# Kernel optimization log

Measured on AMD Instinct MI355X. Metric: run time of the kernel, lower is better.

## Reference

```python
import jax, jax.numpy as jnp
import numpy as np

# physics constants of the two-reaction model
K1 = 1.0
BETA = 16.0
F = 0.1
VR = 1.0
DELTA = 0.01  # sample_time
NG = 3

B, T = 4096, 256
NU, NYS, NUS = 1, 9, 3  # u dim, yseq dim (=(Np-1)*Ng), useq dim (=(Np-1)*Nu)
H = 64
FIN = NG + NYS + NUS  # 15


def setup_inputs() -> dict:
    key = jax.random.key(0)
    ks = jax.random.split(key, 8)
    return {
        "u": jax.random.uniform(ks[0], (B, T, NU), dtype=jnp.float32),
        "yseq": jax.random.uniform(ks[1], (B, T, NYS), dtype=jnp.float32),
        "useq": jax.random.uniform(ks[2], (B, T, NUS), dtype=jnp.float32),
        "W1": 0.1 * jax.random.normal(ks[3], (FIN, H), dtype=jnp.float32),
        "b1": jnp.zeros((H,), jnp.float32),
        "W2": 0.1 * jax.random.normal(ks[4], (H, H), dtype=jnp.float32),
        "b2": jnp.zeros((H,), jnp.float32),
        "W3": 0.1 * jax.random.normal(ks[5], (H, NG), dtype=jnp.float32),
        "b3": jnp.zeros((NG,), jnp.float32),
    }


def _fg(x, u):
    # RHS of the two-reaction ODE; x: (B, 3), u: (B, 1)
    Ca, Cd, Cc = x[..., 0:1], x[..., 1:2], x[..., 2:3]
    Ca0 = u[..., 0:1]
    s = jnp.sqrt(1.0 + BETA * Ca)
    dCa = F * (Ca0 - Ca) / VR - K1 * Ca
    dCd = 0.5 * K1 * Ca * (s - 1.0) / (s + 1.0) - F * Cd / VR
    dCc = 2.0 * K1 * Ca / (1.0 + s) - F * Cc / VR
    return jnp.concatenate([dCa, dCd, dCc], axis=-1)


def reference(u, yseq, useq, W1, b1, W2, b2, W3, b3):
    def fnn(x, ys, us):
        h = jnp.concatenate([x, ys, us], axis=-1)
        h = jax.nn.relu(h @ W1 + b1)
        h = jax.nn.relu(h @ W2 + b2)
        return h @ W3 + b3

    def step(xG, inp):
        u_t, ys_t, us_t = inp
        rhs = lambda x: _fg(x, u_t) + fnn(x, ys_t, us_t)
        k1 = rhs(xG)
        k2 = rhs(xG + 0.5 * DELTA * k1)
        k3 = rhs(xG + 0.5 * DELTA * k2)
        k4 = rhs(xG + DELTA * k3)
        xnext = xG + (DELTA / 6.0) * (k1 + 2.0 * k2 + 2.0 * k3 + k4)
        return xnext, xG  # output y = current state

    x0 = jnp.zeros((u.shape[0], NG), u.dtype)
    xs = (jnp.moveaxis(u, 1, 0), jnp.moveaxis(yseq, 1, 0), jnp.moveaxis(useq, 1, 0))
    _, ys_out = jax.lax.scan(step, x0, xs)
    return jnp.moveaxis(ys_out, 0, 1)  # (B, T, Ng)
```

## Files before the change

kernel.cpp:

```cpp
#include <hip/hip_runtime.h>

#define NB 4096
#define NT 256
#define NH 64


template <int ctrl, int rm, int bm>
__device__ __forceinline__ float dpp_add(float v) {
    int m = __builtin_amdgcn_update_dpp(0, __builtin_bit_cast(int, v),
                                        ctrl, rm, bm, true);
    return v + __builtin_bit_cast(float, m);
}

__device__ __forceinline__ float wave_sum(float v) {
    v = dpp_add<0x111, 0xf, 0xf>(v);
    v = dpp_add<0x112, 0xf, 0xf>(v);
    v = dpp_add<0x114, 0xf, 0xe>(v);
    v = dpp_add<0x118, 0xf, 0xc>(v);
    v = dpp_add<0x142, 0xa, 0xf>(v);
    v = dpp_add<0x143, 0xc, 0xf>(v);
    return __builtin_bit_cast(float,
        __builtin_amdgcn_readlane(__builtin_bit_cast(int, v), 63));
}

__global__ __attribute__((amdgpu_flat_work_group_size(256, 256),
                          amdgpu_waves_per_eu(4, 4)))
void tworeac_kernel(
    const float* __restrict__ u, const float* __restrict__ yseq,
    const float* __restrict__ useq, const float* __restrict__ W1,
    const float* __restrict__ b1, const float* __restrict__ W2,
    const float* __restrict__ b2, const float* __restrict__ W3,
    const float* __restrict__ b3, float* __restrict__ out)
{
    const int lane = threadIdx.x & 63;
    const int wave = threadIdx.x >> 6;
    const int b = blockIdx.x * 4 + wave;

    __shared__ float h1s[4][NH];

    float w1x[3], w1y[9], w1u[3], w2r[NH], w3r[3];
    #pragma unroll
    for (int i = 0; i < 3; ++i) w1x[i] = W1[i * NH + lane];
    #pragma unroll
    for (int i = 0; i < 9; ++i) w1y[i] = W1[(3 + i) * NH + lane];
    #pragma unroll
    for (int i = 0; i < 3; ++i) w1u[i] = W1[(12 + i) * NH + lane];
    #pragma unroll
    for (int j = 0; j < NH; ++j) w2r[j] = W2[j * NH + lane];
    #pragma unroll
    for (int k = 0; k < 3; ++k) w3r[k] = W3[lane * 3 + k];
    #pragma unroll
    for (int j = 0; j < NH; ++j) asm volatile("" : "+v"(w2r[j]));

    const float b1h = b1[lane];
    const float b2h = b2[lane];
    const float b30 = b3[0], b31 = b3[1], b32 = b3[2];

    const float* ub  = u    + (size_t)b * NT;
    const float* ysb = yseq + (size_t)b * NT * 9;
    const float* usb = useq + (size_t)b * NT * 3;
    float*       ob  = out  + (size_t)b * NT * 3;

    float x0 = 0.f, x1 = 0.f, x2 = 0.f;

    float base1 = 0.f, ut = 0.f;
    auto rhs = [&](float xa, float xd, float xc,
                   float& d0, float& d1, float& d2) {
        float h1 = fmaf(xa, w1x[0], fmaf(xd, w1x[1], fmaf(xc, w1x[2], base1)));
        h1 = fmaxf(h1, 0.f);
        h1s[wave][lane] = h1;
        __builtin_amdgcn_wave_barrier();
        float a0 = 0.f, a1 = 0.f, a2 = 0.f, a3 = 0.f;
        #pragma unroll
        for (int j = 0; j < NH / 4; ++j) {
            float4 hv = *reinterpret_cast<const float4*>(&h1s[wave][4 * j]);
            a0 = fmaf(hv.x, w2r[4 * j + 0], a0);
            a1 = fmaf(hv.y, w2r[4 * j + 1], a1);
            a2 = fmaf(hv.z, w2r[4 * j + 2], a2);
            a3 = fmaf(hv.w, w2r[4 * j + 3], a3);
        }
        __builtin_amdgcn_wave_barrier();
        float h2 = fmaxf(b2h + ((a0 + a1) + (a2 + a3)), 0.f);
        float s0 = wave_sum(h2 * w3r[0]);
        float s1 = wave_sum(h2 * w3r[1]);
        float s2 = wave_sum(h2 * w3r[2]);
        float s = sqrtf(fmaf(16.f, xa, 1.f));
        float r = 1.f / (1.f + s);
        d0 = (fmaf(0.1f, ut - xa, -xa)) + s0 + b30;
        d1 = fmaf(0.5f * xa * (s - 1.f), r, -0.1f * xd) + s1 + b31;
        d2 = (2.f * xa * r - 0.1f * xc) + s2 + b32;
    };

    for (int t = 0; t < NT; ++t) {
        if (lane < 3) ob[t * 3 + lane] = (lane == 0) ? x0 : (lane == 1 ? x1 : x2);

        ut = ub[t];
        base1 = b1h;
        #pragma unroll
        for (int i = 0; i < 9; ++i) base1 = fmaf(ysb[t * 9 + i], w1y[i], base1);
        #pragma unroll
        for (int i = 0; i < 3; ++i) base1 = fmaf(usb[t * 3 + i], w1u[i], base1);

        float k0, k1v, k2v, a0, a1, a2;
        rhs(x0, x1, x2, k0, k1v, k2v);
        a0 = k0; a1 = k1v; a2 = k2v;
        rhs(fmaf(0.005f, k0, x0), fmaf(0.005f, k1v, x1),
            fmaf(0.005f, k2v, x2), k0, k1v, k2v);
        a0 = fmaf(2.f, k0, a0); a1 = fmaf(2.f, k1v, a1); a2 = fmaf(2.f, k2v, a2);
        rhs(fmaf(0.005f, k0, x0), fmaf(0.005f, k1v, x1),
            fmaf(0.005f, k2v, x2), k0, k1v, k2v);
        a0 = fmaf(2.f, k0, a0); a1 = fmaf(2.f, k1v, a1); a2 = fmaf(2.f, k2v, a2);
        rhs(fmaf(0.01f, k0, x0), fmaf(0.01f, k1v, x1),
            fmaf(0.01f, k2v, x2), k0, k1v, k2v);
        a0 += k0; a1 += k1v; a2 += k2v;

        const float c = 0.01f / 6.f;
        x0 = fmaf(c, a0, x0);
        x1 = fmaf(c, a1, x1);
        x2 = fmaf(c, a2, x2);
    }
}

extern "C" void kernel_launch(void* const* d_in, const int* in_sizes, int n_in,
                              void* d_out, int out_size, void* d_ws, size_t ws_size,
                              hipStream_t stream) {
    const float* u    = (const float*)d_in[0];
    const float* yseq = (const float*)d_in[1];
    const float* useq = (const float*)d_in[2];
    const float* W1   = (const float*)d_in[3];
    const float* b1   = (const float*)d_in[4];
    const float* W2   = (const float*)d_in[5];
    const float* b2   = (const float*)d_in[6];
    const float* W3   = (const float*)d_in[7];
    const float* b3   = (const float*)d_in[8];
    float* out = (float*)d_out;

    tworeac_kernel<<<NB / 4, 256, 0, stream>>>(u, yseq, useq, W1, b1, W2, b2,
                                               W3, b3, out);
}
```

Measured before the change: 1.187 ms.

## Process two batch chains per wave with packed FP32 math and interleaved reductions

Each wave now integrates two independent batch rows at once, halving the grid. The layer-2 matvec uses packed two-wide float math against the shared W2 registers, and the six wave reductions are interleaved to hide DPP latency. The sqrt and reciprocal calls become the fast hardware intrinsics. The aim is more instruction-level parallelism in the latency-bound serial RK4 chain, at the cost of fewer waves and more registers, with the occupancy hint relaxed to allow that.

```diff
diff --git a/kernel.cpp b/kernel.cpp
--- a/kernel.cpp
+++ b/kernel.cpp
@@ -2,7 +2,8 @@
 
 #define NB 4096
 #define NT 256
-#define NH 64
+
+typedef float f32x2 __attribute__((ext_vector_type(2)));
 
 
 template <int ctrl, int rm, int bm>
@@ -12,19 +13,13 @@
     return v + __builtin_bit_cast(float, m);
 }
 
-__device__ __forceinline__ float wave_sum(float v) {
-    v = dpp_add<0x111, 0xf, 0xf>(v);
-    v = dpp_add<0x112, 0xf, 0xf>(v);
-    v = dpp_add<0x114, 0xf, 0xe>(v);
-    v = dpp_add<0x118, 0xf, 0xc>(v);
-    v = dpp_add<0x142, 0xa, 0xf>(v);
-    v = dpp_add<0x143, 0xc, 0xf>(v);
+__device__ __forceinline__ float rl63(float v) {
     return __builtin_bit_cast(float,
         __builtin_amdgcn_readlane(__builtin_bit_cast(int, v), 63));
 }
 
 __global__ __attribute__((amdgpu_flat_work_group_size(256, 256),
-                          amdgpu_waves_per_eu(4, 4)))
+                          amdgpu_waves_per_eu(2, 4)))
 void tworeac_kernel(
     const float* __restrict__ u, const float* __restrict__ yseq,
     const float* __restrict__ useq, const float* __restrict__ W1,
@@ -34,90 +29,143 @@
 {
     const int lane = threadIdx.x & 63;
     const int wave = threadIdx.x >> 6;
-    const int b = blockIdx.x * 4 + wave;
+    const int cA = (blockIdx.x * 4 + wave) * 2;
+    const int cB = cA + 1;
 
-    __shared__ float h1s[4][NH];
+    __shared__ float h1A[4][64];
+    __shared__ float h1B[4][64];
 
-    float w1x[3], w1y[9], w1u[3], w2r[NH], w3r[3];
+    f32x2 w2p[32];
     #pragma unroll
-    for (int i = 0; i < 3; ++i) w1x[i] = W1[i * NH + lane];
+    for (int m = 0; m < 32; ++m)
+        w2p[m] = (f32x2){W2[(2 * m) * 64 + lane], W2[(2 * m + 1) * 64 + lane]};
+    float w1x[3], w1y[9], w1u[3], w3r[3];
     #pragma unroll
-    for (int i = 0; i < 9; ++i) w1y[i] = W1[(3 + i) * NH + lane];
+    for (int i = 0; i < 3; ++i) w1x[i] = W1[i * 64 + lane];
     #pragma unroll
-    for (int i = 0; i < 3; ++i) w1u[i] = W1[(12 + i) * NH + lane];
+    for (int i = 0; i < 9; ++i) w1y[i] = W1[(3 + i) * 64 + lane];
     #pragma unroll
-    for (int j = 0; j < NH; ++j) w2r[j] = W2[j * NH + lane];
+    for (int i = 0; i < 3; ++i) w1u[i] = W1[(12 + i) * 64 + lane];
     #pragma unroll
     for (int k = 0; k < 3; ++k) w3r[k] = W3[lane * 3 + k];
-    #pragma unroll
-    for (int j = 0; j < NH; ++j) asm volatile("" : "+v"(w2r[j]));
-
     const float b1h = b1[lane];
     const float b2h = b2[lane];
     const float b30 = b3[0], b31 = b3[1], b32 = b3[2];
 
-    const float* ub  = u    + (size_t)b * NT;
-    const float* ysb = yseq + (size_t)b * NT * 9;
-    const float* usb = useq + (size_t)b * NT * 3;
-    float*       ob  = out  + (size_t)b * NT * 3;
+    const float* uA  = u    + (size_t)cA * NT;
+    const float* uB  = u    + (size_t)cB * NT;
+    const float* ysA = yseq + (size_t)cA * NT * 9;
+    const float* ysB = yseq + (size_t)cB * NT * 9;
+    const float* usA = useq + (size_t)cA * NT * 3;
+    const float* usB = useq + (size_t)cB * NT * 3;
+    float*       oA  = out  + (size_t)cA * NT * 3;
+    float*       oB  = out  + (size_t)cB * NT * 3;
 
-    float x0 = 0.f, x1 = 0.f, x2 = 0.f;
+    f32x2 x0p = (f32x2)0.f, x1p = (f32x2)0.f, x2p = (f32x2)0.f;
 
-    float base1 = 0.f, ut = 0.f;
-    auto rhs = [&](float xa, float xd, float xc,
-                   float& d0, float& d1, float& d2) {
-        float h1 = fmaf(xa, w1x[0], fmaf(xd, w1x[1], fmaf(xc, w1x[2], base1)));
-        h1 = fmaxf(h1, 0.f);
-        h1s[wave][lane] = h1;
+    f32x2 basep = (f32x2)0.f;
+    float utA = 0.f, utB = 0.f;
+
+    auto rhs = [&](f32x2 X0, f32x2 X1, f32x2 X2,
+                   f32x2& D0, f32x2& D1, f32x2& D2) {
+        f32x2 h1 = basep + X0 * w1x[0] + X1 * w1x[1] + X2 * w1x[2];
+        h1.x = fmaxf(h1.x, 0.f);
+        h1.y = fmaxf(h1.y, 0.f);
+        h1A[wave][lane] = h1.x;
+        h1B[wave][lane] = h1.y;
         __builtin_amdgcn_wave_barrier();
-        float a0 = 0.f, a1 = 0.f, a2 = 0.f, a3 = 0.f;
+        f32x2 aA0 = (f32x2)0.f, aA1 = (f32x2)0.f;
+        f32x2 aB0 = (f32x2)0.f, aB1 = (f32x2)0.f;
+        const float4* hA4 = reinterpret_cast<const float4*>(&h1A[wave][0]);
+        const float4* hB4 = reinterpret_cast<const float4*>(&h1B[wave][0]);
         #pragma unroll
-        for (int j = 0; j < NH / 4; ++j) {
-            float4 hv = *reinterpret_cast<const float4*>(&h1s[wave][4 * j]);
-            a0 = fmaf(hv.x, w2r[4 * j + 0], a0);
-            a1 = fmaf(hv.y, w2r[4 * j + 1], a1);
-            a2 = fmaf(hv.z, w2r[4 * j + 2], a2);
-            a3 = fmaf(hv.w, w2r[4 * j + 3], a3);
+        for (int jj = 0; jj < 16; ++jj) {
+            float4 qa = hA4[jj];
+            aA0 += (f32x2){qa.x, qa.y} * w2p[2 * jj];
+            aA1 += (f32x2){qa.z, qa.w} * w2p[2 * jj + 1];
+            float4 qb = hB4[jj];
+            aB0 += (f32x2){qb.x, qb.y} * w2p[2 * jj];
+            aB1 += (f32x2){qb.z, qb.w} * w2p[2 * jj + 1];
         }
         __builtin_amdgcn_wave_barrier();
-        float h2 = fmaxf(b2h + ((a0 + a1) + (a2 + a3)), 0.f);
-        float s0 = wave_sum(h2 * w3r[0]);
-        float s1 = wave_sum(h2 * w3r[1]);
-        float s2 = wave_sum(h2 * w3r[2]);
-        float s = sqrtf(fmaf(16.f, xa, 1.f));
-        float r = 1.f / (1.f + s);
-        d0 = (fmaf(0.1f, ut - xa, -xa)) + s0 + b30;
-        d1 = fmaf(0.5f * xa * (s - 1.f), r, -0.1f * xd) + s1 + b31;
-        d2 = (2.f * xa * r - 0.1f * xc) + s2 + b32;
+        float h2A = fmaxf(b2h + ((aA0.x + aA1.x) + (aA0.y + aA1.y)), 0.f);
+        float h2B = fmaxf(b2h + ((aB0.x + aB1.x) + (aB0.y + aB1.y)), 0.f);
+        float q0 = h2A * w3r[0], q1 = h2B * w3r[0];
+        float q2 = h2A * w3r[1], q3 = h2B * w3r[1];
+        float q4 = h2A * w3r[2], q5 = h2B * w3r[2];
+        #define BLVL(CT, RM, BM)                                         \
+            q0 = dpp_add<CT, RM, BM>(q0); q1 = dpp_add<CT, RM, BM>(q1);  \
+            q2 = dpp_add<CT, RM, BM>(q2); q3 = dpp_add<CT, RM, BM>(q3);  \
+            q4 = dpp_add<CT, RM, BM>(q4); q5 = dpp_add<CT, RM, BM>(q5);
+        BLVL(0x111, 0xf, 0xf)
+        BLVL(0x112, 0xf, 0xf)
+        BLVL(0x114, 0xf, 0xe)
+        BLVL(0x118, 0xf, 0xc)
+        BLVL(0x142, 0xa, 0xf)
+        BLVL(0x143, 0xc, 0xf)
+        #undef BLVL
+        float sA0 = rl63(q0), sB0 = rl63(q1);
+        float sA1 = rl63(q2), sB1 = rl63(q3);
+        float sA2 = rl63(q4), sB2 = rl63(q5);
+        float sa = __builtin_amdgcn_sqrtf(fmaf(16.f, X0.x, 1.f));
+        float ra = __builtin_amdgcn_rcpf(1.f + sa);
+        float f0a = fmaf(0.1f, utA - X0.x, -X0.x);
+        float f1a = fmaf(0.5f * X0.x * (sa - 1.f), ra, -0.1f * X1.x);
+        float f2a = fmaf(2.f * X0.x, ra, -0.1f * X2.x);
+        float sb = __builtin_amdgcn_sqrtf(fmaf(16.f, X0.y, 1.f));
+        float rb = __builtin_amdgcn_rcpf(1.f + sb);
+        float f0b = fmaf(0.1f, utB - X0.y, -X0.y);
+        float f1b = fmaf(0.5f * X0.y * (sb - 1.f), rb, -0.1f * X1.y);
+        float f2b = fmaf(2.f * X0.y, rb, -0.1f * X2.y);
+        D0 = (f32x2){(f0a + b30) + sA0, (f0b + b30) + sB0};
+        D1 = (f32x2){(f1a + b31) + sA1, (f1b + b31) + sB1};
+        D2 = (f32x2){(f2a + b32) + sA2, (f2b + b32) + sB2};
     };
 
     for (int t = 0; t < NT; ++t) {
-        if (lane < 3) ob[t * 3 + lane] = (lane == 0) ? x0 : (lane == 1 ? x1 : x2);
+        if (lane < 3) {
+            float v = (lane == 0) ? x0p.x : (lane == 1 ? x1p.x : x2p.x);
+            oA[t * 3 + lane] = v;
+        }
+        {
+            unsigned l2 = (unsigned)(lane - 16);
+            if (l2 < 3u) {
+                float v = (l2 == 0) ? x0p.y : (l2 == 1 ? x1p.y : x2p.y);
+                oB[t * 3 + l2] = v;
+            }
+        }
 
-        ut = ub[t];
-        base1 = b1h;
+        utA = uA[t]; utB = uB[t];
+        float bA = b1h, bB = b1h;
         #pragma unroll
-        for (int i = 0; i < 9; ++i) base1 = fmaf(ysb[t * 9 + i], w1y[i], base1);
+        for (int i = 0; i < 9; ++i) {
+            bA = fmaf(ysA[t * 9 + i], w1y[i], bA);
+            bB = fmaf(ysB[t * 9 + i], w1y[i], bB);
+        }
         #pragma unroll
-        for (int i = 0; i < 3; ++i) base1 = fmaf(usb[t * 3 + i], w1u[i], base1);
+        for (int i = 0; i < 3; ++i) {
+            bA = fmaf(usA[t * 3 + i], w1u[i], bA);
+            bB = fmaf(usB[t * 3 + i], w1u[i], bB);
+        }
+        basep = (f32x2){bA, bB};
 
-        float k0, k1v, k2v, a0, a1, a2;
-        rhs(x0, x1, x2, k0, k1v, k2v);
-        a0 = k0; a1 = k1v; a2 = k2v;
-        rhs(fmaf(0.005f, k0, x0), fmaf(0.005f, k1v, x1),
-            fmaf(0.005f, k2v, x2), k0, k1v, k2v);
-        a0 = fmaf(2.f, k0, a0); a1 = fmaf(2.f, k1v, a1); a2 = fmaf(2.f, k2v, a2);
-        rhs(fmaf(0.005f, k0, x0), fmaf(0.005f, k1v, x1),
-            fmaf(0.005f, k2v, x2), k0, k1v, k2v);
-        a0 = fmaf(2.f, k0, a0); a1 = fmaf(2.f, k1v, a1); a2 = fmaf(2.f, k2v, a2);
-        rhs(fmaf(0.01f, k0, x0), fmaf(0.01f, k1v, x1),
-            fmaf(0.01f, k2v, x2), k0, k1v, k2v);
-        a0 += k0; a1 += k1v; a2 += k2v;
+        f32x2 k0, k1, k2, a0, a1, a2;
+        rhs(x0p, x1p, x2p, k0, k1, k2);
+        a0 = k0; a1 = k1; a2 = k2;
+        rhs(x0p + 0.005f * k0, x1p + 0.005f * k1,
+            x2p + 0.005f * k2, k0, k1, k2);
+        a0 += 2.f * k0; a1 += 2.f * k1; a2 += 2.f * k2;
+        rhs(x0p + 0.005f * k0, x1p + 0.005f * k1,
+            x2p + 0.005f * k2, k0, k1, k2);
+        a0 += 2.f * k0; a1 += 2.f * k1; a2 += 2.f * k2;
+        rhs(x0p + 0.01f * k0, x1p + 0.01f * k1,
+            x2p + 0.01f * k2, k0, k1, k2);
+        a0 += k0; a1 += k1; a2 += k2;
 
         const float c = 0.01f / 6.f;
-        x0 = fmaf(c, a0, x0);
-        x1 = fmaf(c, a1, x1);
-        x2 = fmaf(c, a2, x2);
+        x0p += c * a0;
+        x1p += c * a1;
+        x2p += c * a2;
     }
 }
 
@@ -135,6 +183,6 @@
     const float* b3   = (const float*)d_in[8];
     float* out = (float*)d_out;
 
-    tworeac_kernel<<<NB / 4, 256, 0, stream>>>(u, yseq, useq, W1, b1, W2, b2,
+    tworeac_kernel<<<NB / 8, 256, 0, stream>>>(u, yseq, useq, W1, b1, W2, b2,
                                                W3, b3, out);
 }
```

New measurement: 1.426 ms. 20.1% more time.
